# Kernel optimization log

Hardware: AMD Instinct MI355X
Metric: run time of the kernel (lower is better)

## Reference

```python
import jax, jax.numpy as jnp
import numpy as np

B, H, L, D = 2, 16, 2048, 64


def setup_inputs() -> dict:
    key = jax.random.key(0)
    kq, kk, kv = jax.random.split(key, 3)
    q = jax.random.normal(kq, (B, H, L, D), dtype=jnp.float32)
    k = jax.random.normal(kk, (B, H, L, D), dtype=jnp.float32)
    v = jax.random.normal(kv, (B, H, L, D), dtype=jnp.float32)
    return {"q": q, "k": k, "v": v}


def reference(q, k, v):
    use_norm = True
    seq_len = q.shape[-2]
    scale = q.shape[-1] ** (-0.5)
    q = q * scale
    # [B, H, L, L] score matrix
    attn = jnp.einsum("bhqd,bhkd->bhqk", q, k)
    # 2nd-order Taylor expansion of exp: 1 + s + 0.5*s^2
    attn = 1.0 + attn + 0.5 * attn * attn
    # causal mask (lower-triangular kept)
    causal = jnp.tril(jnp.ones((seq_len, seq_len), dtype=bool))
    attn = jnp.where(causal, attn, 0.0)
    o = jnp.einsum("bhqk,bhkd->bhqd", attn, v)
    if use_norm:
        z = attn.sum(-1)
        o = o / (z[..., None] + 1e-06)
    return o
```

## Files before the change

### kernel.cpp

```cpp
#include <hip/hip_runtime.h>
#include <hip/hip_bf16.h>

typedef __bf16    bf16x8  __attribute__((ext_vector_type(8)));
typedef __bf16    bf16x4  __attribute__((ext_vector_type(4)));
typedef _Float16  half8   __attribute__((ext_vector_type(8)));
typedef _Float16  half4   __attribute__((ext_vector_type(4)));
typedef _Float16  half2   __attribute__((ext_vector_type(2)));
typedef float     floatx4 __attribute__((ext_vector_type(4)));

constexpr int Bc  = 2;
constexpr int Hc  = 16;
constexpr int Lc  = 2048;
constexpr int Dc  = 64;
constexpr int BHn = Bc * Hc;
constexpr int BM  = 128;
constexpr int BN  = 128;
constexpr int NQT = Lc / BM;
constexpr int LDK = 72;
constexpr int LDV = 136;

static __device__ __forceinline__ half2 pack_f16(float a, float b) {
    return __builtin_bit_cast(half2, __builtin_amdgcn_cvt_pkrtz(a, b));
}

__global__ void prep(const float* __restrict__ kp, const float* __restrict__ vp,
                     __bf16* __restrict__ k16, _Float16* __restrict__ v16) {
    const int bid = blockIdx.x, tid = threadIdx.x;
    if (bid < 1024) {
        const size_t base = (size_t)bid * 4096 + tid * 4;
        #pragma unroll
        for (int rep = 0; rep < 4; ++rep) {
            const size_t i = base + rep * 1024;
            floatx4 v = *(const floatx4*)(kp + i);
            bf16x4 b;
            b[0] = (__bf16)v[0]; b[1] = (__bf16)v[1]; b[2] = (__bf16)v[2]; b[3] = (__bf16)v[3];
            *(bf16x4*)(k16 + i) = b;
        }
    } else {
        const int vb  = bid - 1024;
        const int bh  = vb >> 5, kt = vb & 31;
        const int key = kt * 64 + (tid & 63);
        const int k5  = key & 31;
        const int pcol = (key & ~31) | (((k5 >> 2) & 3) * 8 + ((k5 >> 4) & 1) * 4 + (k5 & 3));
        const int d0  = (tid >> 6) * 16;
        const float* src = vp + ((size_t)bh * Lc + key) * Dc;
        _Float16*    dst = v16 + (size_t)bh * Dc * Lc + pcol;
        #pragma unroll
        for (int i = 0; i < 16; ++i) {
            const int d = d0 + i;
            dst[(size_t)d * Lc] = (_Float16)src[d];
        }
    }
}

__global__ __launch_bounds__(256, 2)
void taylor_attn(const float* __restrict__ qp, const __bf16* __restrict__ k16,
                 const _Float16* __restrict__ v16, float* __restrict__ op)
{
    __shared__ __bf16   Ks[BN * LDK];
    __shared__ _Float16 VT[Dc * LDV];

    const int tid  = threadIdx.x;
    const int wv   = tid >> 6;
    const int lane = tid & 63;
    const int lm   = lane & 15;
    const int quad = lane >> 4;

    const int cu    = (int)(blockIdx.x & 255);
    const int snd   = (int)(blockIdx.x >> 8);
    const int bh    = cu & 31;
    const int qslot = cu >> 5;
    const int qi    = snd ? qslot : (NQT - 1 - qslot);
    const int q0    = qi * BM;
    const int jmax  = qi;

    const float*    qbase = qp  + ((size_t)bh * Lc + q0) * Dc;
    const __bf16*   kj    = k16 + (size_t)bh * Lc * Dc;
    const _Float16* vj    = v16 + (size_t)bh * Dc * Lc;

    bf16x8 kr[4]; half8 vr[4];
    #pragma unroll
    for (int rep = 0; rep < 4; ++rep)
        kr[rep] = *(const bf16x8*)(kj + 8 * (tid + 256 * rep));
    #pragma unroll
    for (int rep = 0; rep < 4; ++rep) {
        const int g = tid + 256 * rep;
        vr[rep] = *(const half8*)(vj + (size_t)(g >> 4) * Lc + (g & 15) * 8);
    }

    {
        const int r0 = tid >> 4, c4 = tid & 15;
        #pragma unroll
        for (int rep = 0; rep < 8; ++rep) {
            const int row = r0 + rep * 16;
            floatx4 v = *(const floatx4*)(qbase + row * Dc + c4 * 4);
            bf16x4 b;
            b[0] = (__bf16)v[0]; b[1] = (__bf16)v[1]; b[2] = (__bf16)v[2]; b[3] = (__bf16)v[3];
            *(bf16x4*)&Ks[row * LDK + c4 * 4] = b;
        }
    }
    __syncthreads();
    bf16x8 qa[2][2];
    #pragma unroll
    for (int st = 0; st < 2; ++st)
        #pragma unroll
        for (int kf = 0; kf < 2; ++kf)
            qa[st][kf] = *(const bf16x8*)&Ks[(32 * wv + 16 * st + lm) * LDK + kf * 32 + quad * 8];
    __syncthreads();

    floatx4 oacc[2][4] = {};
    floatx4 zacc[2]    = {};

    const half8 ones = {(_Float16)1.f, (_Float16)1.f, (_Float16)1.f, (_Float16)1.f,
                        (_Float16)1.f, (_Float16)1.f, (_Float16)1.f, (_Float16)1.f};
    const half2 c8  = {(_Float16)0.125f, (_Float16)0.125f};
    const half2 c1  = {(_Float16)1.f,    (_Float16)1.f};
    const half2 ch  = {(_Float16)0.5f,   (_Float16)0.5f};

    for (int j = 0; j <= jmax; ++j) {
        #pragma unroll
        for (int rep = 0; rep < 4; ++rep) {
            const int c = tid + 256 * rep;
            *(bf16x8*)&Ks[(c >> 3) * LDK + (c & 7) * 8] = kr[rep];
        }
        #pragma unroll
        for (int rep = 0; rep < 4; ++rep) {
            const int g = tid + 256 * rep;
            *(half8*)&VT[(g >> 4) * LDV + (g & 15) * 8] = vr[rep];
        }
        __syncthreads();

        if (j < jmax) {
            kj += BN * Dc;
            vj += BN;
            #pragma unroll
            for (int rep = 0; rep < 4; ++rep)
                kr[rep] = *(const bf16x8*)(kj + 8 * (tid + 256 * rep));
            #pragma unroll
            for (int rep = 0; rep < 4; ++rep) {
                const int g = tid + 256 * rep;
                vr[rep] = *(const half8*)(vj + (size_t)(g >> 4) * Lc + (g & 15) * 8);
            }
        }

        const bool nm = (j == jmax);
        #pragma unroll
        for (int half = 0; half < 2; ++half) {
            floatx4 sacc[2][4] = {};
            #pragma unroll
            for (int kb4 = 0; kb4 < 4; ++kb4) {
                const int kb = 4 * half + kb4;
                #pragma unroll
                for (int kf = 0; kf < 2; ++kf) {
                    bf16x8 ka = *(const bf16x8*)&Ks[(16 * kb + lm) * LDK + kf * 32 + quad * 8];
                    sacc[0][kb4] = __builtin_amdgcn_mfma_f32_16x16x32_bf16(ka, qa[0][kf], sacc[0][kb4], 0, 0, 0);
                    sacc[1][kb4] = __builtin_amdgcn_mfma_f32_16x16x32_bf16(ka, qa[1][kf], sacc[1][kb4], 0, 0, 0);
                }
            }

            half8 wf[2][2];
            #pragma unroll
            for (int st = 0; st < 2; ++st) {
                const int strip_lo = q0 + 32 * wv + 16 * st;
                const int thr = strip_lo + lm - j * BN;
                half2 wh[4][2];
                #pragma unroll
                for (int kb4 = 0; kb4 < 4; ++kb4) {
                    half2 s01 = pack_f16(sacc[st][kb4][0], sacc[st][kb4][1]);
                    half2 s23 = pack_f16(sacc[st][kb4][2], sacc[st][kb4][3]);
                    half2 a01 = s01 * c8 + c1;
                    half2 a23 = s23 * c8 + c1;
                    half2 w01 = a01 * (a01 * ch) + ch;
                    half2 w23 = a23 * (a23 * ch) + ch;
                    if (nm) {
                        const int i0 = 16 * (4 * half + kb4) + 4 * quad;
                        w01[0] = (i0 + 0 <= thr) ? w01[0] : (_Float16)0.f;
                        w01[1] = (i0 + 1 <= thr) ? w01[1] : (_Float16)0.f;
                        w23[0] = (i0 + 2 <= thr) ? w23[0] : (_Float16)0.f;
                        w23[1] = (i0 + 3 <= thr) ? w23[1] : (_Float16)0.f;
                    }
                    wh[kb4][0] = w01;
                    wh[kb4][1] = w23;
                }
                #pragma unroll
                for (int g2 = 0; g2 < 2; ++g2) {
                    half4 lo = __builtin_shufflevector(wh[2 * g2][0],     wh[2 * g2][1],     0, 1, 2, 3);
                    half4 hi = __builtin_shufflevector(wh[2 * g2 + 1][0], wh[2 * g2 + 1][1], 0, 1, 2, 3);
                    wf[st][g2] = __builtin_shufflevector(lo, hi, 0, 1, 2, 3, 4, 5, 6, 7);
                }
            }

            #pragma unroll
            for (int db = 0; db < 4; ++db)
                #pragma unroll
                for (int g2 = 0; g2 < 2; ++g2) {
                    const int grp = 2 * half + g2;
                    half8 va = *(const half8*)&VT[(16 * db + lm) * LDV + 32 * grp + 8 * quad];
                    oacc[0][db] = __builtin_amdgcn_mfma_f32_16x16x32_f16(va, wf[0][g2], oacc[0][db], 0, 0, 0);
                    oacc[1][db] = __builtin_amdgcn_mfma_f32_16x16x32_f16(va, wf[1][g2], oacc[1][db], 0, 0, 0);
                }
            #pragma unroll
            for (int g2 = 0; g2 < 2; ++g2) {
                zacc[0] = __builtin_amdgcn_mfma_f32_16x16x32_f16(ones, wf[0][g2], zacc[0], 0, 0, 0);
                zacc[1] = __builtin_amdgcn_mfma_f32_16x16x32_f16(ones, wf[1][g2], zacc[1], 0, 0, 0);
            }
        }
        __syncthreads();
    }

    #pragma unroll
    for (int st = 0; st < 2; ++st) {
        const float inv = 1.0f / (zacc[st][0] + 1e-6f);
        const int qrow = q0 + 32 * wv + 16 * st + lm;
        float* orow = op + ((size_t)bh * Lc + qrow) * Dc;
        #pragma unroll
        for (int db = 0; db < 4; ++db)
            #pragma unroll
            for (int r = 0; r < 4; ++r)
                orow[16 * db + 4 * quad + r] = oacc[st][db][r] * inv;
    }
}

extern "C" void kernel_launch(void* const* d_in, const int* in_sizes, int n_in,
                              void* d_out, int out_size, void* d_ws, size_t ws_size,
                              hipStream_t stream) {
    const float* q = (const float*)d_in[0];
    const float* k = (const float*)d_in[1];
    const float* v = (const float*)d_in[2];
    float* o = (float*)d_out;

    __bf16*   k16 = (__bf16*)d_ws;
    _Float16* v16 = (_Float16*)((char*)d_ws + (size_t)BHn * Lc * Dc * 2);

    prep<<<dim3(2048), dim3(256), 0, stream>>>(k, v, k16, v16);
    taylor_attn<<<dim3(NQT * BHn), dim3(256), 0, stream>>>(q, k16, v16, o);
}
```

Measured before the change: 119.6 us.

## Split waves 2x2 over query and key halves with shared-memory output reduction

Remaps the four waves from each owning 32 query rows across all 128 keys to a 2x2 grid: two query groups of 64 rows times two key halves of 64 keys. Each K and V fragment read from LDS now feeds four MFMAs instead of two, which halves LDS read traffic per tile. The two key-half partial outputs and normalizers are combined through shared memory at the end, and the final store is vectorized to floatx4. In exchange, accumulator register use doubles and an extra reduction pass with a barrier is added, which may pressure occupancy.

```diff
diff --git a/kernel.cpp b/kernel.cpp
--- a/kernel.cpp
+++ b/kernel.cpp
@@ -18,6 +18,7 @@
 constexpr int NQT = Lc / BM;
 constexpr int LDK = 72;
 constexpr int LDV = 136;
+constexpr int SMEM_BYTES = 35840;
 
 static __device__ __forceinline__ half2 pack_f16(float a, float b) {
     return __builtin_bit_cast(half2, __builtin_amdgcn_cvt_pkrtz(a, b));
@@ -57,14 +58,17 @@
 void taylor_attn(const float* __restrict__ qp, const __bf16* __restrict__ k16,
                  const _Float16* __restrict__ v16, float* __restrict__ op)
 {
-    __shared__ __bf16   Ks[BN * LDK];
-    __shared__ _Float16 VT[Dc * LDV];
+    __shared__ __align__(16) char smem[SMEM_BYTES];
+    __bf16*   Ks = (__bf16*)smem;
+    _Float16* VT = (_Float16*)(smem + 18432);
 
     const int tid  = threadIdx.x;
     const int wv   = tid >> 6;
     const int lane = tid & 63;
     const int lm   = lane & 15;
     const int quad = lane >> 4;
+    const int wq   = wv >> 1;
+    const int wk   = wv & 1;
 
     const int cu    = (int)(blockIdx.x & 255);
     const int snd   = (int)(blockIdx.x >> 8);
@@ -100,16 +104,16 @@
         }
     }
     __syncthreads();
-    bf16x8 qa[2][2];
+    bf16x8 qa[4][2];
     #pragma unroll
-    for (int st = 0; st < 2; ++st)
+    for (int st = 0; st < 4; ++st)
         #pragma unroll
         for (int kf = 0; kf < 2; ++kf)
-            qa[st][kf] = *(const bf16x8*)&Ks[(32 * wv + 16 * st + lm) * LDK + kf * 32 + quad * 8];
+            qa[st][kf] = *(const bf16x8*)&Ks[(64 * wq + 16 * st + lm) * LDK + kf * 32 + quad * 8];
     __syncthreads();
 
-    floatx4 oacc[2][4] = {};
-    floatx4 zacc[2]    = {};
+    floatx4 oacc[4][4] = {};
+    floatx4 zacc[4]    = {};
 
     const half8 ones = {(_Float16)1.f, (_Float16)1.f, (_Float16)1.f, (_Float16)1.f,
                         (_Float16)1.f, (_Float16)1.f, (_Float16)1.f, (_Float16)1.f};
@@ -145,27 +149,29 @@
 
         const bool nm = (j == jmax);
         #pragma unroll
-        for (int half = 0; half < 2; ++half) {
-            floatx4 sacc[2][4] = {};
-            #pragma unroll
-            for (int kb4 = 0; kb4 < 4; ++kb4) {
-                const int kb = 4 * half + kb4;
+        for (int hf = 0; hf < 2; ++hf) {
+            const int grp = 2 * wk + hf;
+
+            floatx4 sacc[4][2] = {};
+            #pragma unroll
+            for (int kb4 = 0; kb4 < 2; ++kb4) {
+                const int row0 = 16 * (4 * wk + 2 * hf + kb4);
                 #pragma unroll
                 for (int kf = 0; kf < 2; ++kf) {
-                    bf16x8 ka = *(const bf16x8*)&Ks[(16 * kb + lm) * LDK + kf * 32 + quad * 8];
-                    sacc[0][kb4] = __builtin_amdgcn_mfma_f32_16x16x32_bf16(ka, qa[0][kf], sacc[0][kb4], 0, 0, 0);
-                    sacc[1][kb4] = __builtin_amdgcn_mfma_f32_16x16x32_bf16(ka, qa[1][kf], sacc[1][kb4], 0, 0, 0);
+                    bf16x8 ka = *(const bf16x8*)&Ks[(row0 + lm) * LDK + kf * 32 + quad * 8];
+                    #pragma unroll
+                    for (int st = 0; st < 4; ++st)
+                        sacc[st][kb4] = __builtin_amdgcn_mfma_f32_16x16x32_bf16(ka, qa[st][kf], sacc[st][kb4], 0, 0, 0);
                 }
             }
 
-            half8 wf[2][2];
-            #pragma unroll
-            for (int st = 0; st < 2; ++st) {
-                const int strip_lo = q0 + 32 * wv + 16 * st;
-                const int thr = strip_lo + lm - j * BN;
-                half2 wh[4][2];
+            half8 wf[4];
+            #pragma unroll
+            for (int st = 0; st < 4; ++st) {
+                const int thr = q0 + 64 * wq + 16 * st + lm - j * BN;
+                half2 wh[2][2];
                 #pragma unroll
-                for (int kb4 = 0; kb4 < 4; ++kb4) {
+                for (int kb4 = 0; kb4 < 2; ++kb4) {
                     half2 s01 = pack_f16(sacc[st][kb4][0], sacc[st][kb4][1]);
                     half2 s23 = pack_f16(sacc[st][kb4][2], sacc[st][kb4][3]);
                     half2 a01 = s01 * c8 + c1;
@@ -173,7 +179,7 @@
                     half2 w01 = a01 * (a01 * ch) + ch;
                     half2 w23 = a23 * (a23 * ch) + ch;
                     if (nm) {
-                        const int i0 = 16 * (4 * half + kb4) + 4 * quad;
+                        const int i0 = 16 * (4 * wk + 2 * hf + kb4) + 4 * quad;
                         w01[0] = (i0 + 0 <= thr) ? w01[0] : (_Float16)0.f;
                         w01[1] = (i0 + 1 <= thr) ? w01[1] : (_Float16)0.f;
                         w23[0] = (i0 + 2 <= thr) ? w23[0] : (_Float16)0.f;
@@ -182,42 +188,52 @@
                     wh[kb4][0] = w01;
                     wh[kb4][1] = w23;
                 }
+                half4 lo = __builtin_shufflevector(wh[0][0], wh[0][1], 0, 1, 2, 3);
+                half4 hi = __builtin_shufflevector(wh[1][0], wh[1][1], 0, 1, 2, 3);
+                wf[st] = __builtin_shufflevector(lo, hi, 0, 1, 2, 3, 4, 5, 6, 7);
+            }
+
+            #pragma unroll
+            for (int db = 0; db < 4; ++db) {
+                half8 va = *(const half8*)&VT[(16 * db + lm) * LDV + 32 * grp + 8 * quad];
                 #pragma unroll
-                for (int g2 = 0; g2 < 2; ++g2) {
-                    half4 lo = __builtin_shufflevector(wh[2 * g2][0],     wh[2 * g2][1],     0, 1, 2, 3);
-                    half4 hi = __builtin_shufflevector(wh[2 * g2 + 1][0], wh[2 * g2 + 1][1], 0, 1, 2, 3);
-                    wf[st][g2] = __builtin_shufflevector(lo, hi, 0, 1, 2, 3, 4, 5, 6, 7);
-                }
-            }
-
+                for (int st = 0; st < 4; ++st)
+                    oacc[st][db] = __builtin_amdgcn_mfma_f32_16x16x32_f16(va, wf[st], oacc[st][db], 0, 0, 0);
+            }
+            #pragma unroll
+            for (int st = 0; st < 4; ++st)
+                zacc[st] = __builtin_amdgcn_mfma_f32_16x16x32_f16(ones, wf[st], zacc[st], 0, 0, 0);
+        }
+        __syncthreads();
+    }
+
+    float* Ored = (float*)smem;
+    float* zred = (float*)(smem + 34816);
+    if (wk) {
+        #pragma unroll
+        for (int st = 0; st < 4; ++st) {
+            const int r = wq * 64 + 16 * st + lm;
             #pragma unroll
             for (int db = 0; db < 4; ++db)
-                #pragma unroll
-                for (int g2 = 0; g2 < 2; ++g2) {
-                    const int grp = 2 * half + g2;
-                    half8 va = *(const half8*)&VT[(16 * db + lm) * LDV + 32 * grp + 8 * quad];
-                    oacc[0][db] = __builtin_amdgcn_mfma_f32_16x16x32_f16(va, wf[0][g2], oacc[0][db], 0, 0, 0);
-                    oacc[1][db] = __builtin_amdgcn_mfma_f32_16x16x32_f16(va, wf[1][g2], oacc[1][db], 0, 0, 0);
-                }
-            #pragma unroll
-            for (int g2 = 0; g2 < 2; ++g2) {
-                zacc[0] = __builtin_amdgcn_mfma_f32_16x16x32_f16(ones, wf[0][g2], zacc[0], 0, 0, 0);
-                zacc[1] = __builtin_amdgcn_mfma_f32_16x16x32_f16(ones, wf[1][g2], zacc[1], 0, 0, 0);
-            }
-        }
-        __syncthreads();
-    }
-
-    #pragma unroll
-    for (int st = 0; st < 2; ++st) {
-        const float inv = 1.0f / (zacc[st][0] + 1e-6f);
-        const int qrow = q0 + 32 * wv + 16 * st + lm;
-        float* orow = op + ((size_t)bh * Lc + qrow) * Dc;
-        #pragma unroll
-        for (int db = 0; db < 4; ++db)
-            #pragma unroll
-            for (int r = 0; r < 4; ++r)
-                orow[16 * db + 4 * quad + r] = oacc[st][db][r] * inv;
+                *(floatx4*)&Ored[(size_t)r * 68 + 16 * db + 4 * quad] = oacc[st][db];
+            zred[r] = zacc[st][0];
+        }
+    }
+    __syncthreads();
+    if (!wk) {
+        #pragma unroll
+        for (int st = 0; st < 4; ++st) {
+            const int r = wq * 64 + 16 * st + lm;
+            const float inv = 1.0f / (zacc[st][0] + zred[r] + 1e-6f);
+            const int qrow = q0 + 64 * wq + 16 * st + lm;
+            float* orow = op + ((size_t)bh * Lc + qrow) * Dc;
+            #pragma unroll
+            for (int db = 0; db < 4; ++db) {
+                floatx4 part = *(const floatx4*)&Ored[(size_t)r * 68 + 16 * db + 4 * quad];
+                floatx4 t = (oacc[st][db] + part) * inv;
+                *(floatx4*)&orow[16 * db + 4 * quad] = t;
+            }
+        }
     }
 }
 
```

Result: no change. 118.3 us (-1.1%).
